# Performance work log

Measured on AMD Instinct MI355X. Metric: run time of the kernel, lower is better.

## Reference

```python
import jax, jax.numpy as jnp
import numpy as np
from jax.ops import segment_sum, segment_max

N_NODES = 16384
N_EDGES = 262144
NODE_DIM = 480
HIDDEN = 256
OUT_DIM = 128
HEADS = 4
N_GRAPHS = 256


def setup_inputs() -> dict:
    key = jax.random.key(0)
    ks = jax.random.split(key, 40)
    p = {}
    p['x'] = jax.random.normal(ks[0], (N_NODES, NODE_DIM), jnp.float32)
    p['edge_index'] = jax.random.randint(ks[1], (2, N_EDGES), 0, N_NODES)
    p['edge_attr'] = jax.random.uniform(ks[2], (N_EDGES, 1), dtype=jnp.float32)
    p['batch'] = jnp.sort(jax.random.randint(ks[3], (N_NODES,), 0, N_GRAPHS))
    p['num_graphs'] = N_GRAPHS
    def w(k, shape):
        return jax.random.normal(k, shape, jnp.float32) * 0.05
    i = 4
    for l, (din, h, c) in zip((1, 2, 3), [(NODE_DIM, HEADS, HIDDEN // HEADS), (HIDDEN, HEADS, HIDDEN // HEADS), (HIDDEN, 1, OUT_DIM)]):
        dout = h * c
        p[f'Wl{l}'] = w(ks[i], (din, dout)); i += 1
        p[f'bl{l}'] = jnp.zeros((dout,), jnp.float32)
        p[f'Wr{l}'] = w(ks[i], (din, dout)); i += 1
        p[f'br{l}'] = jnp.zeros((dout,), jnp.float32)
        p[f'We{l}'] = w(ks[i], (1, dout)); i += 1
        p[f'att{l}'] = w(ks[i], (h, c)); i += 1
        p[f'bo{l}'] = jnp.zeros((dout,), jnp.float32)
    for l, d in [(1, HIDDEN), (2, HIDDEN), (3, OUT_DIM)]:
        p[f'g{l}'] = jnp.ones((d,), jnp.float32)
        p[f'b{l}'] = jnp.zeros((d,), jnp.float32)
    p['Wres'] = w(ks[i], (NODE_DIM, HIDDEN))
    return p


def _layer_norm(x, g, b):
    mu = x.mean(-1, keepdims=True)
    v = ((x - mu) ** 2).mean(-1, keepdims=True)
    return (x - mu) * jax.lax.rsqrt(v + 1e-5) * g + b


def _gatv2(x, src, dst, ea, Wl, bl, Wr, br, We, att, bias):
    # PyG GATv2Conv, eval mode (dropout off), add_self_loops=True, fill_value='mean'
    N = x.shape[0]
    H, C = att.shape
    # self-loop edge attr = scatter-mean of incoming edge attrs per node
    deg = segment_sum(jnp.ones((src.shape[0],), x.dtype), dst, num_segments=N)
    loop_ea = segment_sum(ea, dst, num_segments=N) / jnp.maximum(deg, 1.0)[:, None]
    ar = jnp.arange(N, dtype=src.dtype)
    src2 = jnp.concatenate([src, ar])
    dst2 = jnp.concatenate([dst, ar])
    ea2 = jnp.concatenate([ea, loop_ea], axis=0)
    xl = (x @ Wl + bl).reshape(N, H, C)
    xr = (x @ Wr + br).reshape(N, H, C)
    e = (ea2 @ We).reshape(-1, H, C)
    m = jax.nn.leaky_relu(xl[src2] + xr[dst2] + e, 0.2)  # [E', H, C]
    alpha = jnp.einsum('ehc,hc->eh', m, att)
    amax = segment_max(alpha, dst2, num_segments=N)  # [N, H]; every node has a self loop
    ex = jnp.exp(alpha - amax[dst2])
    denom = segment_sum(ex, dst2, num_segments=N)
    a = ex / denom[dst2]
    out = segment_sum(a[:, :, None] * xl[src2], dst2, num_segments=N)  # [N, H, C]
    return out.reshape(N, H * C) + bias


def _forward(x, edge_attr, params, edge_index, batch, num_graphs):
    (Wl1, bl1, Wr1, br1, We1, att1, bo1,
     Wl2, bl2, Wr2, br2, We2, att2, bo2,
     Wl3, bl3, Wr3, br3, We3, att3, bo3,
     g1, b1, g2, b2, g3, b3, Wres) = params
    src, dst = edge_index[0], edge_index[1]
    gelu = lambda t: jax.nn.gelu(t, approximate=False)
    h = gelu(_layer_norm(_gatv2(x, src, dst, edge_attr, Wl1, bl1, Wr1, br1, We1, att1, bo1), g1, b1))
    h = h + x @ Wres
    h2 = gelu(_layer_norm(_gatv2(h, src, dst, edge_attr, Wl2, bl2, Wr2, br2, We2, att2, bo2), g2, b2))
    h2 = h2 + h
    h3 = _layer_norm(_gatv2(h2, src, dst, edge_attr, Wl3, bl3, Wr3, br3, We3, att3, bo3), g3, b3)
    # global mean pool over graphs
    sums = segment_sum(h3, batch, num_segments=num_graphs)
    cnt = segment_sum(jnp.ones((h3.shape[0],), h3.dtype), batch, num_segments=num_graphs)
    return sums / jnp.maximum(cnt, 1.0)[:, None]


def reference(x, edge_index, edge_attr, batch, num_graphs,
              Wl1, bl1, Wr1, br1, We1, att1, bo1,
              Wl2, bl2, Wr2, br2, We2, att2, bo2,
              Wl3, bl3, Wr3, br3, We3, att3, bo3,
              g1, b1, g2, b2, g3, b3, Wres):
    params = (Wl1, bl1, Wr1, br1, We1, att1, bo1,
              Wl2, bl2, Wr2, br2, We2, att2, bo2,
              Wl3, bl3, Wr3, br3, We3, att3, bo3,
              g1, b1, g2, b2, g3, b3, Wres)
    return _forward(x, edge_attr, params, edge_index, batch, num_graphs)
```

## Files before the change

kernel.cpp:

```cpp
#include <hip/hip_runtime.h>
#include <hip/hip_bf16.h>
#include <math.h>

#define NN 16384
#define NE 262144
#define KDIM1 480
#define DHID 256
#define DOUT3 128
#define NG 256

typedef short bf16x8 __attribute__((ext_vector_type(8)));
typedef float f32x4 __attribute__((ext_vector_type(4)));

#define LOG2E 1.44269504088896340736f

__device__ __forceinline__ unsigned short f2bf(float f) {
  unsigned u = __float_as_uint(f);
  unsigned r = (u + 0x7fffu + ((u >> 16) & 1u)) >> 16;
  return (unsigned short)r;
}
__device__ __forceinline__ float bf2f(unsigned short u) {
  return __uint_as_float((unsigned)u << 16);
}

__device__ __forceinline__ void gload_lds16(const void* g, void* l) {
  __builtin_amdgcn_global_load_lds((const __attribute__((address_space(1))) void*)g,
                                   (__attribute__((address_space(3))) void*)l,
                                   16, 0, 0);
}


__global__ __launch_bounds__(256) void k_edge_count(const int* __restrict__ ei,
                                                    const float* __restrict__ ea,
                                                    int* __restrict__ deg,
                                                    float* __restrict__ easum) {
  int e = blockIdx.x * 256 + threadIdx.x;
  if (e >= NE) return;
  int d = ei[NE + e];
  atomicAdd(&deg[d], 1);
  atomicAdd(&easum[d], ea[e]);
}

__global__ __launch_bounds__(1024) void k_scan(const int* __restrict__ deg,
                                               float* __restrict__ easum,
                                               int* __restrict__ offs,
                                               int* __restrict__ cursor) {
  __shared__ int sums[1024];
  int t = threadIdx.x;
  int base = t * 16;
  int local[16];
  int s = 0;
#pragma unroll
  for (int i = 0; i < 16; ++i) { local[i] = deg[base + i]; s += local[i]; }
  sums[t] = s;
  __syncthreads();
  for (int d = 1; d < 1024; d <<= 1) {
    int v = (t >= d) ? sums[t - d] : 0;
    __syncthreads();
    sums[t] += v;
    __syncthreads();
  }
  int prefix = (t == 0) ? 0 : sums[t - 1];
#pragma unroll
  for (int i = 0; i < 16; ++i) {
    offs[base + i] = prefix;
    cursor[base + i] = prefix;
    prefix += local[i];
  }
  if (t == 1023) offs[NN] = prefix;
#pragma unroll
  for (int i = 0; i < 16; ++i) {
    easum[base + i] = easum[base + i] / fmaxf((float)local[i], 1.f);
  }
}

__global__ __launch_bounds__(256) void k_fill_csr(const int* __restrict__ ei,
                                                  const float* __restrict__ ea,
                                                  int* __restrict__ cursor,
                                                  int* __restrict__ csr_src,
                                                  float* __restrict__ csr_ea) {
  int e = blockIdx.x * 256 + threadIdx.x;
  if (e >= NE) return;
  int s = ei[e];
  int d = ei[NE + e];
  int pos = atomicAdd(&cursor[d], 1);
  csr_src[pos] = s;
  csr_ea[pos] = ea[e];
}


#define PREP_S0 (NN * KDIM1 / 4)
#define PREP_S1 (2 * DHID * KDIM1)
#define PREP_S2 (DHID * KDIM1)
#define PREP_S3 (2 * DHID * DHID)
#define PREP_S4 (2 * DOUT3 * DHID)
#define PREP_TOTAL (PREP_S0 + PREP_S1 + PREP_S2 + PREP_S3 + PREP_S4)

__global__ __launch_bounds__(256) void k_prep(
    const float* __restrict__ x,
    const float* __restrict__ Wl1, const float* __restrict__ Wr1,
    const float* __restrict__ Wres,
    const float* __restrict__ Wl2, const float* __restrict__ Wr2,
    const float* __restrict__ Wl3, const float* __restrict__ Wr3,
    unsigned short* __restrict__ actb0, unsigned short* __restrict__ Wc1,
    unsigned short* __restrict__ Wrs, unsigned short* __restrict__ Wc2,
    unsigned short* __restrict__ Wc3) {
  int idx = blockIdx.x * 256 + threadIdx.x;
  if (idx < PREP_S0) {
    int i = idx * 4;
    float4 v = *(const float4*)&x[i];
    ushort4 o;
    o.x = f2bf(v.x); o.y = f2bf(v.y); o.z = f2bf(v.z); o.w = f2bf(v.w);
    *(ushort4*)&actb0[i] = o;
    return;
  }
  idx -= PREP_S0;
  if (idx < PREP_S1) {
    int n = idx / KDIM1, k = idx % KDIM1;
    float v = (n < DHID) ? Wl1[(size_t)k * DHID + n] : Wr1[(size_t)k * DHID + (n - DHID)];
    Wc1[idx] = f2bf(v);
    return;
  }
  idx -= PREP_S1;
  if (idx < PREP_S2) {
    int n = idx / KDIM1, k = idx % KDIM1;
    Wrs[idx] = f2bf(Wres[(size_t)k * DHID + n]);
    return;
  }
  idx -= PREP_S2;
  if (idx < PREP_S3) {
    int n = idx / DHID, k = idx % DHID;
    float v = (n < DHID) ? Wl2[(size_t)k * DHID + n] : Wr2[(size_t)k * DHID + (n - DHID)];
    Wc2[idx] = f2bf(v);
    return;
  }
  idx -= PREP_S3;
  if (idx < PREP_S4) {
    int n = idx / DHID, k = idx % DHID;
    float v = (n < DOUT3) ? Wl3[(size_t)k * DOUT3 + n] : Wr3[(size_t)k * DOUT3 + (n - DOUT3)];
    Wc3[idx] = f2bf(v);
  }
}


#define GEMM_CORE128(A_, Bt_, K_)                                                \
  __shared__ short As[128 * 32];                                                 \
  __shared__ short Bs[128 * 32];                                                 \
  int t = threadIdx.x;                                                           \
  int w = t >> 6;                                                                \
  int lane = t & 63;                                                             \
  int bm = blockIdx.y * 128;                                                     \
  int bn = blockIdx.x * 128;                                                     \
  int wr = w >> 1, wc = w & 1;                                                   \
  const short* Ag0 = A_ + (size_t)(bm + w * 16 + (lane >> 2)) * K_ + (lane & 3) * 8;        \
  const short* Ag1 = A_ + (size_t)(bm + 64 + w * 16 + (lane >> 2)) * K_ + (lane & 3) * 8;   \
  const short* Bg0 = Bt_ + (size_t)(bn + w * 16 + (lane >> 2)) * K_ + (lane & 3) * 8;       \
  const short* Bg1 = Bt_ + (size_t)(bn + 64 + w * 16 + (lane >> 2)) * K_ + (lane & 3) * 8;  \
  short* Al0 = &As[w * 16 * 32];                                                 \
  short* Al1 = &As[(64 + w * 16) * 32];                                          \
  short* Bl0 = &Bs[w * 16 * 32];                                                 \
  short* Bl1 = &Bs[(64 + w * 16) * 32];                                          \
  f32x4 acc[4][4] = {};                                                          \
  for (int k0 = 0; k0 < K_; k0 += 32) {                                          \
    gload_lds16(Ag0, Al0);                                                       \
    gload_lds16(Ag1, Al1);                                                       \
    gload_lds16(Bg0, Bl0);                                                       \
    gload_lds16(Bg1, Bl1);                                                       \
    Ag0 += 32; Ag1 += 32; Bg0 += 32; Bg1 += 32;                                  \
    __syncthreads();                                                             \
    bf16x8 af[4], bfv[4];                                                        \
    _Pragma("unroll")                                                            \
    for (int mi = 0; mi < 4; ++mi)                                               \
      af[mi] = *(const bf16x8*)&As[(wr * 64 + mi * 16 + (lane & 15)) * 32 + (lane >> 4) * 8]; \
    _Pragma("unroll")                                                            \
    for (int ni = 0; ni < 4; ++ni)                                               \
      bfv[ni] = *(const bf16x8*)&Bs[(wc * 64 + ni * 16 + (lane & 15)) * 32 + (lane >> 4) * 8]; \
    _Pragma("unroll")                                                            \
    for (int mi = 0; mi < 4; ++mi)                                               \
      _Pragma("unroll")                                                          \
      for (int ni = 0; ni < 4; ++ni)                                             \
        acc[mi][ni] = __builtin_amdgcn_mfma_f32_16x16x32_bf16(af[mi], bfv[ni], acc[mi][ni], 0, 0, 0); \
    __syncthreads();                                                             \
  }                                                                              \
  int col = lane & 15;                                                           \
  int row4 = (lane >> 4) * 4;

__global__ __launch_bounds__(256) void gemm_lr(const short* __restrict__ A,
                                               const short* __restrict__ Wt,
                                               const float* __restrict__ bl,
                                               const float* __restrict__ br,
                                               unsigned short* __restrict__ xlb,
                                               unsigned short* __restrict__ xrb,
                                               int K, int NH) {
  GEMM_CORE128(A, Wt, K)
  bool right = (bn >= NH);
  unsigned short* outp = right ? xrb : xlb;
  const float* bias = right ? br : bl;
  int cbase = right ? bn - NH : bn;
#pragma unroll
  for (int mi = 0; mi < 4; ++mi) {
#pragma unroll
    for (int ni = 0; ni < 4; ++ni) {
      f32x4 a = acc[mi][ni];
      int gc = cbase + wc * 64 + ni * 16 + col;
      float bv = bias[gc];
#pragma unroll
      for (int r = 0; r < 4; ++r) {
        int gr = bm + wr * 64 + mi * 16 + row4 + r;
        outp[(size_t)gr * NH + gc] = f2bf(a[r] + bv);
      }
    }
  }
}

__global__ __launch_bounds__(256) void gemm_res(const short* __restrict__ A,
                                                const short* __restrict__ Wt,
                                                float* __restrict__ Cf,
                                                unsigned short* __restrict__ outb,
                                                int K, int N) {
  GEMM_CORE128(A, Wt, K)
#pragma unroll
  for (int mi = 0; mi < 4; ++mi) {
#pragma unroll
    for (int ni = 0; ni < 4; ++ni) {
      f32x4 a = acc[mi][ni];
      int gc = bn + wc * 64 + ni * 16 + col;
#pragma unroll
      for (int r = 0; r < 4; ++r) {
        int gr = bm + wr * 64 + mi * 16 + row4 + r;
        size_t o = (size_t)gr * N + gc;
        float v = a[r] + Cf[o];
        Cf[o] = v;
        outb[o] = f2bf(v);
      }
    }
  }
}


template<int D, int H, bool GELU_, bool RES_, bool WF32, bool WBF16>
__global__ __launch_bounds__(256) void gat_fused(
    const unsigned short* __restrict__ xlb, const unsigned short* __restrict__ xrb,
    const float* __restrict__ We, const float* __restrict__ att,
    const float* __restrict__ bo,
    const int* __restrict__ offs, const int* __restrict__ csr_src,
    const float* __restrict__ csr_ea, const float* __restrict__ loop_ea,
    const float* __restrict__ g, const float* __restrict__ bln,
    const float* __restrict__ res,
    float* __restrict__ outf, unsigned short* __restrict__ outb) {
  constexpr int P = D / 64;
  constexpr int C = D / H;
  constexpr int GROUP = C / P;
  int n = (blockIdx.x * blockDim.x + threadIdx.x) >> 6;
  int lane = threadIdx.x & 63;
  if (n >= NN) return;
  int d0 = lane * P;

  float wev[P], attv[P], xrv[P];
  if constexpr (P == 4) {
    *(float4*)wev = *(const float4*)&We[d0];
    *(float4*)attv = *(const float4*)&att[d0];
    ushort4 u = *(const ushort4*)&xrb[(size_t)n * D + d0];
    xrv[0] = bf2f(u.x); xrv[1] = bf2f(u.y); xrv[2] = bf2f(u.z); xrv[3] = bf2f(u.w);
  } else {
    *(float2*)wev = *(const float2*)&We[d0];
    *(float2*)attv = *(const float2*)&att[d0];
    ushort2 u = *(const ushort2*)&xrb[(size_t)n * D + d0];
    xrv[0] = bf2f(u.x); xrv[1] = bf2f(u.y);
  }
#pragma unroll
  for (int p = 0; p < P; ++p) attv[p] *= LOG2E;

#define GATHER(dst, srcidx)                                                  \
  {                                                                          \
    if constexpr (P == 4) {                                                  \
      ushort4 u_ = *(const ushort4*)&xlb[(size_t)(srcidx) * D + d0];         \
      dst[0] = bf2f(u_.x); dst[1] = bf2f(u_.y);                              \
      dst[2] = bf2f(u_.z); dst[3] = bf2f(u_.w);                              \
    } else {                                                                 \
      ushort2 u_ = *(const ushort2*)&xlb[(size_t)(srcidx) * D + d0];         \
      dst[0] = bf2f(u_.x); dst[1] = bf2f(u_.y);                              \
    }                                                                        \
  }

#define ALPHA(out_, xv_, eav_)                                               \
  {                                                                          \
    float partial_ = 0.f;                                                    \
    _Pragma("unroll")                                                        \
    for (int p = 0; p < P; ++p) {                                            \
      float s_ = xv_[p] + xrv[p] + (eav_) * wev[p];                          \
      s_ = fmaxf(s_, 0.2f * s_);                                             \
      partial_ = fmaf(s_, attv[p], partial_);                                \
    }                                                                        \
    _Pragma("unroll")                                                        \
    for (int w_ = 1; w_ < GROUP; w_ <<= 1) partial_ += __shfl_xor(partial_, w_, 64); \
    out_ = partial_;                                                         \
  }

  float acc[P];
  float xs[P];
  GATHER(xs, n)
  float m;
  ALPHA(m, xs, loop_ea[n])
  float l = 1.f;
#pragma unroll
  for (int p = 0; p < P; ++p) acc[p] = xs[p];

  int beg = offs[n];
  int cnt = offs[n + 1] - beg;
  int sbeg = __builtin_amdgcn_readfirstlane(beg);
  int scnt = __builtin_amdgcn_readfirstlane(cnt);

  int e = 0;
  for (; e + 4 <= scnt; e += 4) {
    int src0 = csr_src[sbeg + e];
    int src1 = csr_src[sbeg + e + 1];
    int src2 = csr_src[sbeg + e + 2];
    int src3 = csr_src[sbeg + e + 3];
    float ea0 = csr_ea[sbeg + e];
    float ea1 = csr_ea[sbeg + e + 1];
    float ea2 = csr_ea[sbeg + e + 2];
    float ea3 = csr_ea[sbeg + e + 3];
    float xv0[P], xv1[P], xv2[P], xv3[P];
    GATHER(xv0, src0)
    GATHER(xv1, src1)
    GATHER(xv2, src2)
    GATHER(xv3, src3)
    float a0, a1, a2, a3;
    ALPHA(a0, xv0, ea0)
    ALPHA(a1, xv1, ea1)
    ALPHA(a2, xv2, ea2)
    ALPHA(a3, xv3, ea3)
    float nm = fmaxf(fmaxf(m, fmaxf(a0, a1)), fmaxf(a2, a3));
    float sc = exp2f(m - nm);
    float pe0 = exp2f(a0 - nm);
    float pe1 = exp2f(a1 - nm);
    float pe2 = exp2f(a2 - nm);
    float pe3 = exp2f(a3 - nm);
    l = fmaf(l, sc, (pe0 + pe1) + (pe2 + pe3));
#pragma unroll
    for (int p = 0; p < P; ++p)
      acc[p] = fmaf(acc[p], sc,
                    fmaf(pe0, xv0[p], fmaf(pe1, xv1[p], fmaf(pe2, xv2[p], pe3 * xv3[p]))));
    m = nm;
  }
  for (; e < scnt; ++e) {
    int src0 = csr_src[sbeg + e];
    float ea0 = csr_ea[sbeg + e];
    float xv0[P];
    GATHER(xv0, src0)
    float a0;
    ALPHA(a0, xv0, ea0)
    float nm = fmaxf(m, a0);
    float sc = exp2f(m - nm);
    float pe0 = exp2f(a0 - nm);
    l = fmaf(l, sc, pe0);
#pragma unroll
    for (int p = 0; p < P; ++p) acc[p] = fmaf(acc[p], sc, pe0 * xv0[p]);
    m = nm;
  }
#undef GATHER
#undef ALPHA

  float inv = 1.f / l;
  float y[P];
#pragma unroll
  for (int p = 0; p < P; ++p) y[p] = fmaf(acc[p], inv, bo[d0 + p]);

  float s = 0.f, s2 = 0.f;
#pragma unroll
  for (int p = 0; p < P; ++p) { s += y[p]; s2 = fmaf(y[p], y[p], s2); }
#pragma unroll
  for (int w = 1; w < 64; w <<= 1) {
    s += __shfl_xor(s, w, 64);
    s2 += __shfl_xor(s2, w, 64);
  }
  float mu = s * (1.f / D);
  float var = s2 * (1.f / D) - mu * mu;
  float rr = rsqrtf(var + 1e-5f);

  float z[P];
#pragma unroll
  for (int p = 0; p < P; ++p) {
    float v = (y[p] - mu) * rr * g[d0 + p] + bln[d0 + p];
    if (GELU_) v = 0.5f * v * (1.f + erff(v * 0.70710678118654752f));
    if (RES_) v += res[(size_t)n * D + d0 + p];
    z[p] = v;
  }
  if (WF32) {
    float* orow = outf + (size_t)n * D;
    if constexpr (P == 4) *(float4*)&orow[d0] = *(float4*)z;
    else                  *(float2*)&orow[d0] = *(float2*)z;
  }
  if (WBF16) {
    unsigned short* orow = outb + (size_t)n * D;
    if constexpr (P == 4) {
      ushort4 o; o.x = f2bf(z[0]); o.y = f2bf(z[1]); o.z = f2bf(z[2]); o.w = f2bf(z[3]);
      *(ushort4*)&orow[d0] = o;
    } else {
      ushort2 o; o.x = f2bf(z[0]); o.y = f2bf(z[1]);
      *(ushort2*)&orow[d0] = o;
    }
  }
}


__device__ __forceinline__ int lower_bound_i(const int* arr, int n, int val) {
  int lo = 0, hi = n;
  while (lo < hi) {
    int mid = (lo + hi) >> 1;
    if (arr[mid] < val) lo = mid + 1; else hi = mid;
  }
  return lo;
}

__global__ __launch_bounds__(128) void k_pool(const float* __restrict__ h3,
                                              const int* __restrict__ batch,
                                              float* __restrict__ out) {
  int gidx = blockIdx.x;
  int d = threadIdx.x;
  int lo = lower_bound_i(batch, NN, gidx);
  int hi = lower_bound_i(batch, NN, gidx + 1);
  float s = 0.f;
  for (int n = lo; n < hi; ++n) s += h3[(size_t)n * DOUT3 + d];
  int cnt = hi - lo;
  out[gidx * DOUT3 + d] = s / fmaxf((float)cnt, 1.f);
}


extern "C" void kernel_launch(void* const* d_in, const int* in_sizes, int n_in,
                              void* d_out, int out_size, void* d_ws, size_t ws_size,
                              hipStream_t stream) {
  const float* x   = (const float*)d_in[0];
  const int*   ei  = (const int*)d_in[1];
  const float* ea  = (const float*)d_in[2];
  const int*   bat = (const int*)d_in[3];
  const float* Wl1 = (const float*)d_in[5];  const float* bl1 = (const float*)d_in[6];
  const float* Wr1 = (const float*)d_in[7];  const float* br1 = (const float*)d_in[8];
  const float* We1 = (const float*)d_in[9];  const float* at1 = (const float*)d_in[10];
  const float* bo1 = (const float*)d_in[11];
  const float* Wl2 = (const float*)d_in[12]; const float* bl2 = (const float*)d_in[13];
  const float* Wr2 = (const float*)d_in[14]; const float* br2 = (const float*)d_in[15];
  const float* We2 = (const float*)d_in[16]; const float* at2 = (const float*)d_in[17];
  const float* bo2 = (const float*)d_in[18];
  const float* Wl3 = (const float*)d_in[19]; const float* bl3 = (const float*)d_in[20];
  const float* Wr3 = (const float*)d_in[21]; const float* br3 = (const float*)d_in[22];
  const float* We3 = (const float*)d_in[23]; const float* at3 = (const float*)d_in[24];
  const float* bo3 = (const float*)d_in[25];
  const float* g1 = (const float*)d_in[26]; const float* b1 = (const float*)d_in[27];
  const float* g2 = (const float*)d_in[28]; const float* b2 = (const float*)d_in[29];
  const float* g3 = (const float*)d_in[30]; const float* b3 = (const float*)d_in[31];
  const float* Wres = (const float*)d_in[32];
  float* out = (float*)d_out;

  char* ws = (char*)d_ws;
  size_t off = 0;
  int*   deg    = (int*)(ws + off); off += NN * 4;
  float* easum  = (float*)(ws + off); off += NN * 4;
  size_t zero_bytes = off;
  unsigned short* xlb = (unsigned short*)(ws + off); off += (size_t)NN * DHID * 2;
  unsigned short* xrb = (unsigned short*)(ws + off); off += (size_t)NN * DHID * 2;
  float* hb = (float*)(ws + off); off += (size_t)NN * DHID * 4;
  float* h3 = (float*)(ws + off); off += (size_t)NN * DOUT3 * 4;
  unsigned short* actb0 = (unsigned short*)(ws + off); off += (size_t)NN * KDIM1 * 2;
  unsigned short* actb1 = (unsigned short*)(ws + off); off += (size_t)NN * DHID * 2;
  int*   offs   = (int*)(ws + off); off += (NN + 1) * 4 + 60;
  int*   cursor = (int*)(ws + off); off += NN * 4;
  int*   csr_src = (int*)(ws + off); off += (size_t)NE * 4;
  float* csr_ea  = (float*)(ws + off); off += (size_t)NE * 4;
  unsigned short* Wc1 = (unsigned short*)(ws + off); off += (size_t)2 * DHID * KDIM1 * 2;
  unsigned short* Wrs = (unsigned short*)(ws + off); off += (size_t)DHID * KDIM1 * 2;
  unsigned short* Wc2 = (unsigned short*)(ws + off); off += (size_t)2 * DHID * DHID * 2;
  unsigned short* Wc3 = (unsigned short*)(ws + off); off += (size_t)2 * DOUT3 * DHID * 2;

  hipMemsetAsync(deg, 0, zero_bytes, stream);
  k_edge_count<<<NE / 256, 256, 0, stream>>>(ei, ea, deg, easum);
  k_scan<<<1, 1024, 0, stream>>>(deg, easum, offs, cursor);
  k_fill_csr<<<NE / 256, 256, 0, stream>>>(ei, ea, cursor, csr_src, csr_ea);
  k_prep<<<PREP_TOTAL / 256, 256, 0, stream>>>(x, Wl1, Wr1, Wres, Wl2, Wr2, Wl3, Wr3,
                                               actb0, Wc1, Wrs, Wc2, Wc3);

  dim3 blk(256);
  int nwave_blocks = NN / 4;

  gemm_lr<<<dim3(2 * DHID / 128, NN / 128), blk, 0, stream>>>(
      (const short*)actb0, (const short*)Wc1, bl1, br1, xlb, xrb, KDIM1, DHID);
  gat_fused<DHID, 4, true, false, true, false><<<nwave_blocks, blk, 0, stream>>>(
      xlb, xrb, We1, at1, bo1, offs, csr_src, csr_ea, easum, g1, b1, nullptr, hb, nullptr);
  gemm_res<<<dim3(DHID / 128, NN / 128), blk, 0, stream>>>(
      (const short*)actb0, (const short*)Wrs, hb, actb1, KDIM1, DHID);

  gemm_lr<<<dim3(2 * DHID / 128, NN / 128), blk, 0, stream>>>(
      (const short*)actb1, (const short*)Wc2, bl2, br2, xlb, xrb, DHID, DHID);
  gat_fused<DHID, 4, true, true, false, true><<<nwave_blocks, blk, 0, stream>>>(
      xlb, xrb, We2, at2, bo2, offs, csr_src, csr_ea, easum, g2, b2, hb, nullptr, actb1);

  gemm_lr<<<dim3(2 * DOUT3 / 128, NN / 128), blk, 0, stream>>>(
      (const short*)actb1, (const short*)Wc3, bl3, br3, xlb, xrb, DHID, DOUT3);
  gat_fused<DOUT3, 1, false, false, true, false><<<nwave_blocks, blk, 0, stream>>>(
      xlb, xrb, We3, at3, bo3, offs, csr_src, csr_ea, easum, g3, b3, nullptr, h3, nullptr);

  k_pool<<<NG, 128, 0, stream>>>(h3, bat, out);
}
```

Baseline: 263.7 us.

## Fuse residual GEMM into layer-1 GEMM and pooling into layer-3 GAT

The Wres projection is concatenated with Wl1/Wr1 so a single GEMM over the 480-wide input produces xl, xr and the fp32 residual. Layer-1 GAT now adds that residual itself and writes the bf16 activations, which removes the separate gemm_res pass and its second read of actb0. The global mean pool is folded into the layer-3 GAT epilogue through atomic adds scaled by precomputed inverse graph counts, and h3 is no longer written. The cost is heavy atomic contention on the 256x128 output, plus atomic summation order that is not deterministic.

```diff
diff --git a/kernel.cpp b/kernel.cpp
--- a/kernel.cpp
+++ b/kernel.cpp
@@ -27,6 +27,15 @@
   __builtin_amdgcn_global_load_lds((const __attribute__((address_space(1))) void*)g,
                                    (__attribute__((address_space(3))) void*)l,
                                    16, 0, 0);
+}
+
+__device__ __forceinline__ int lower_bound_i(const int* arr, int n, int val) {
+  int lo = 0, hi = n;
+  while (lo < hi) {
+    int mid = (lo + hi) >> 1;
+    if (arr[mid] < val) lo = mid + 1; else hi = mid;
+  }
+  return lo;
 }
 
 
@@ -44,7 +53,9 @@
 __global__ __launch_bounds__(1024) void k_scan(const int* __restrict__ deg,
                                                float* __restrict__ easum,
                                                int* __restrict__ offs,
-                                               int* __restrict__ cursor) {
+                                               int* __restrict__ cursor,
+                                               const int* __restrict__ bat,
+                                               float* __restrict__ ginv) {
   __shared__ int sums[1024];
   int t = threadIdx.x;
   int base = t * 16;
@@ -71,6 +82,11 @@
 #pragma unroll
   for (int i = 0; i < 16; ++i) {
     easum[base + i] = easum[base + i] / fmaxf((float)local[i], 1.f);
+  }
+  if (t < NG) {
+    int lo = lower_bound_i(bat, NN, t);
+    int hi = lower_bound_i(bat, NN, t + 1);
+    ginv[t] = 1.f / fmaxf((float)(hi - lo), 1.f);
   }
 }
 
@@ -90,11 +106,10 @@
 
 
 #define PREP_S0 (NN * KDIM1 / 4)
-#define PREP_S1 (2 * DHID * KDIM1)
-#define PREP_S2 (DHID * KDIM1)
-#define PREP_S3 (2 * DHID * DHID)
-#define PREP_S4 (2 * DOUT3 * DHID)
-#define PREP_TOTAL (PREP_S0 + PREP_S1 + PREP_S2 + PREP_S3 + PREP_S4)
+#define PREP_S1 (3 * DHID * KDIM1)
+#define PREP_S2 (2 * DHID * DHID)
+#define PREP_S3 (2 * DOUT3 * DHID)
+#define PREP_TOTAL (PREP_S0 + PREP_S1 + PREP_S2 + PREP_S3)
 
 __global__ __launch_bounds__(256) void k_prep(
     const float* __restrict__ x,
@@ -102,9 +117,8 @@
     const float* __restrict__ Wres,
     const float* __restrict__ Wl2, const float* __restrict__ Wr2,
     const float* __restrict__ Wl3, const float* __restrict__ Wr3,
-    unsigned short* __restrict__ actb0, unsigned short* __restrict__ Wc1,
-    unsigned short* __restrict__ Wrs, unsigned short* __restrict__ Wc2,
-    unsigned short* __restrict__ Wc3) {
+    unsigned short* __restrict__ actb0, unsigned short* __restrict__ Wc1e,
+    unsigned short* __restrict__ Wc2, unsigned short* __restrict__ Wc3) {
   int idx = blockIdx.x * 256 + threadIdx.x;
   if (idx < PREP_S0) {
     int i = idx * 4;
@@ -117,25 +131,22 @@
   idx -= PREP_S0;
   if (idx < PREP_S1) {
     int n = idx / KDIM1, k = idx % KDIM1;
-    float v = (n < DHID) ? Wl1[(size_t)k * DHID + n] : Wr1[(size_t)k * DHID + (n - DHID)];
-    Wc1[idx] = f2bf(v);
+    float v;
+    if (n < DHID)            v = Wl1[(size_t)k * DHID + n];
+    else if (n < 2 * DHID)   v = Wr1[(size_t)k * DHID + (n - DHID)];
+    else                     v = Wres[(size_t)k * DHID + (n - 2 * DHID)];
+    Wc1e[idx] = f2bf(v);
     return;
   }
   idx -= PREP_S1;
   if (idx < PREP_S2) {
-    int n = idx / KDIM1, k = idx % KDIM1;
-    Wrs[idx] = f2bf(Wres[(size_t)k * DHID + n]);
-    return;
-  }
-  idx -= PREP_S2;
-  if (idx < PREP_S3) {
     int n = idx / DHID, k = idx % DHID;
     float v = (n < DHID) ? Wl2[(size_t)k * DHID + n] : Wr2[(size_t)k * DHID + (n - DHID)];
     Wc2[idx] = f2bf(v);
     return;
   }
-  idx -= PREP_S3;
-  if (idx < PREP_S4) {
+  idx -= PREP_S2;
+  if (idx < PREP_S3) {
     int n = idx / DHID, k = idx % DHID;
     float v = (n < DOUT3) ? Wl3[(size_t)k * DOUT3 + n] : Wr3[(size_t)k * DOUT3 + (n - DOUT3)];
     Wc3[idx] = f2bf(v);
@@ -185,6 +196,43 @@
   int col = lane & 15;                                                           \
   int row4 = (lane >> 4) * 4;
 
+__global__ __launch_bounds__(256) void gemm_lrr(const short* __restrict__ A,
+                                                const short* __restrict__ Wt,
+                                                const float* __restrict__ bl,
+                                                const float* __restrict__ br,
+                                                unsigned short* __restrict__ xlb,
+                                                unsigned short* __restrict__ xrb,
+                                                float* __restrict__ xres,
+                                                int K, int NH) {
+  GEMM_CORE128(A, Wt, K)
+  int seg = bn / NH;
+  int cbase = bn - seg * NH;
+#pragma unroll
+  for (int mi = 0; mi < 4; ++mi) {
+#pragma unroll
+    for (int ni = 0; ni < 4; ++ni) {
+      f32x4 a = acc[mi][ni];
+      int gc = cbase + wc * 64 + ni * 16 + col;
+      if (seg == 2) {
+#pragma unroll
+        for (int r = 0; r < 4; ++r) {
+          int gr = bm + wr * 64 + mi * 16 + row4 + r;
+          xres[(size_t)gr * NH + gc] = a[r];
+        }
+      } else {
+        const float* bias = seg ? br : bl;
+        unsigned short* outp = seg ? xrb : xlb;
+        float bv = bias[gc];
+#pragma unroll
+        for (int r = 0; r < 4; ++r) {
+          int gr = bm + wr * 64 + mi * 16 + row4 + r;
+          outp[(size_t)gr * NH + gc] = f2bf(a[r] + bv);
+        }
+      }
+    }
+  }
+}
+
 __global__ __launch_bounds__(256) void gemm_lr(const short* __restrict__ A,
                                                const short* __restrict__ Wt,
                                                const float* __restrict__ bl,
@@ -213,32 +261,8 @@
   }
 }
 
-__global__ __launch_bounds__(256) void gemm_res(const short* __restrict__ A,
-                                                const short* __restrict__ Wt,
-                                                float* __restrict__ Cf,
-                                                unsigned short* __restrict__ outb,
-                                                int K, int N) {
-  GEMM_CORE128(A, Wt, K)
-#pragma unroll
-  for (int mi = 0; mi < 4; ++mi) {
-#pragma unroll
-    for (int ni = 0; ni < 4; ++ni) {
-      f32x4 a = acc[mi][ni];
-      int gc = bn + wc * 64 + ni * 16 + col;
-#pragma unroll
-      for (int r = 0; r < 4; ++r) {
-        int gr = bm + wr * 64 + mi * 16 + row4 + r;
-        size_t o = (size_t)gr * N + gc;
-        float v = a[r] + Cf[o];
-        Cf[o] = v;
-        outb[o] = f2bf(v);
-      }
-    }
-  }
-}
-
-
-template<int D, int H, bool GELU_, bool RES_, bool WF32, bool WBF16>
+
+template<int D, int H, bool GELU_, bool RES_, bool WF32, bool WBF16, bool POOL>
 __global__ __launch_bounds__(256) void gat_fused(
     const unsigned short* __restrict__ xlb, const unsigned short* __restrict__ xrb,
     const float* __restrict__ We, const float* __restrict__ att,
@@ -247,7 +271,9 @@
     const float* __restrict__ csr_ea, const float* __restrict__ loop_ea,
     const float* __restrict__ g, const float* __restrict__ bln,
     const float* __restrict__ res,
-    float* __restrict__ outf, unsigned short* __restrict__ outb) {
+    float* __restrict__ outf, unsigned short* __restrict__ outb,
+    const int* __restrict__ batch, const float* __restrict__ ginv,
+    float* __restrict__ outp) {
   constexpr int P = D / 64;
   constexpr int C = D / H;
   constexpr int GROUP = C / P;
@@ -402,29 +428,13 @@
       *(ushort2*)&orow[d0] = o;
     }
   }
-}
-
-
-__device__ __forceinline__ int lower_bound_i(const int* arr, int n, int val) {
-  int lo = 0, hi = n;
-  while (lo < hi) {
-    int mid = (lo + hi) >> 1;
-    if (arr[mid] < val) lo = mid + 1; else hi = mid;
-  }
-  return lo;
-}
-
-__global__ __launch_bounds__(128) void k_pool(const float* __restrict__ h3,
-                                              const int* __restrict__ batch,
-                                              float* __restrict__ out) {
-  int gidx = blockIdx.x;
-  int d = threadIdx.x;
-  int lo = lower_bound_i(batch, NN, gidx);
-  int hi = lower_bound_i(batch, NN, gidx + 1);
-  float s = 0.f;
-  for (int n = lo; n < hi; ++n) s += h3[(size_t)n * DOUT3 + d];
-  int cnt = hi - lo;
-  out[gidx * DOUT3 + d] = s / fmaxf((float)cnt, 1.f);
+  if (POOL) {
+    int gr = batch[n];
+    float wgt = ginv[gr];
+#pragma unroll
+    for (int p = 0; p < P; ++p)
+      atomicAdd(&outp[gr * D + d0 + p], z[p] * wgt);
+  }
 }
 
 
@@ -460,45 +470,45 @@
   size_t zero_bytes = off;
   unsigned short* xlb = (unsigned short*)(ws + off); off += (size_t)NN * DHID * 2;
   unsigned short* xrb = (unsigned short*)(ws + off); off += (size_t)NN * DHID * 2;
-  float* hb = (float*)(ws + off); off += (size_t)NN * DHID * 4;
-  float* h3 = (float*)(ws + off); off += (size_t)NN * DOUT3 * 4;
+  float* hb   = (float*)(ws + off); off += (size_t)NN * DHID * 4;
+  float* xres = (float*)(ws + off); off += (size_t)NN * DHID * 4;
   unsigned short* actb0 = (unsigned short*)(ws + off); off += (size_t)NN * KDIM1 * 2;
   unsigned short* actb1 = (unsigned short*)(ws + off); off += (size_t)NN * DHID * 2;
   int*   offs   = (int*)(ws + off); off += (NN + 1) * 4 + 60;
   int*   cursor = (int*)(ws + off); off += NN * 4;
+  float* ginv   = (float*)(ws + off); off += NG * 4;
   int*   csr_src = (int*)(ws + off); off += (size_t)NE * 4;
   float* csr_ea  = (float*)(ws + off); off += (size_t)NE * 4;
-  unsigned short* Wc1 = (unsigned short*)(ws + off); off += (size_t)2 * DHID * KDIM1 * 2;
-  unsigned short* Wrs = (unsigned short*)(ws + off); off += (size_t)DHID * KDIM1 * 2;
-  unsigned short* Wc2 = (unsigned short*)(ws + off); off += (size_t)2 * DHID * DHID * 2;
-  unsigned short* Wc3 = (unsigned short*)(ws + off); off += (size_t)2 * DOUT3 * DHID * 2;
+  unsigned short* Wc1e = (unsigned short*)(ws + off); off += (size_t)3 * DHID * KDIM1 * 2;
+  unsigned short* Wc2  = (unsigned short*)(ws + off); off += (size_t)2 * DHID * DHID * 2;
+  unsigned short* Wc3  = (unsigned short*)(ws + off); off += (size_t)2 * DOUT3 * DHID * 2;
 
   hipMemsetAsync(deg, 0, zero_bytes, stream);
+  hipMemsetAsync(out, 0, (size_t)NG * DOUT3 * 4, stream);
   k_edge_count<<<NE / 256, 256, 0, stream>>>(ei, ea, deg, easum);
-  k_scan<<<1, 1024, 0, stream>>>(deg, easum, offs, cursor);
+  k_scan<<<1, 1024, 0, stream>>>(deg, easum, offs, cursor, bat, ginv);
   k_fill_csr<<<NE / 256, 256, 0, stream>>>(ei, ea, cursor, csr_src, csr_ea);
-  k_prep<<<PREP_TOTAL / 256, 256, 0, stream>>>(x, Wl1, Wr1, Wres, Wl2, Wr2, Wl3, Wr3,
-                                               actb0, Wc1, Wrs, Wc2, Wc3);
+  k_prep<<<(PREP_TOTAL + 255) / 256, 256, 0, stream>>>(x, Wl1, Wr1, Wres, Wl2, Wr2, Wl3, Wr3,
+                                                       actb0, Wc1e, Wc2, Wc3);
 
   dim3 blk(256);
   int nwave_blocks = NN / 4;
 
-  gemm_lr<<<dim3(2 * DHID / 128, NN / 128), blk, 0, stream>>>(
-      (const short*)actb0, (const short*)Wc1, bl1, br1, xlb, xrb, KDIM1, DHID);
-  gat_fused<DHID, 4, true, false, true, false><<<nwave_blocks, blk, 0, stream>>>(
-      xlb, xrb, We1, at1, bo1, offs, csr_src, csr_ea, easum, g1, b1, nullptr, hb, nullptr);
-  gemm_res<<<dim3(DHID / 128, NN / 128), blk, 0, stream>>>(
-      (const short*)actb0, (const short*)Wrs, hb, actb1, KDIM1, DHID);
+  gemm_lrr<<<dim3(3 * DHID / 128, NN / 128), blk, 0, stream>>>(
+      (const short*)actb0, (const short*)Wc1e, bl1, br1, xlb, xrb, xres, KDIM1, DHID);
+  gat_fused<DHID, 4, true, true, true, true, false><<<nwave_blocks, blk, 0, stream>>>(
+      xlb, xrb, We1, at1, bo1, offs, csr_src, csr_ea, easum, g1, b1, xres, hb, actb1,
+      nullptr, nullptr, nullptr);
 
   gemm_lr<<<dim3(2 * DHID / 128, NN / 128), blk, 0, stream>>>(
       (const short*)actb1, (const short*)Wc2, bl2, br2, xlb, xrb, DHID, DHID);
-  gat_fused<DHID, 4, true, true, false, true><<<nwave_blocks, blk, 0, stream>>>(
-      xlb, xrb, We2, at2, bo2, offs, csr_src, csr_ea, easum, g2, b2, hb, nullptr, actb1);
+  gat_fused<DHID, 4, true, true, false, true, false><<<nwave_blocks, blk, 0, stream>>>(
+      xlb, xrb, We2, at2, bo2, offs, csr_src, csr_ea, easum, g2, b2, hb, nullptr, actb1,
+      nullptr, nullptr, nullptr);
 
   gemm_lr<<<dim3(2 * DOUT3 / 128, NN / 128), blk, 0, stream>>>(
       (const short*)actb1, (const short*)Wc3, bl3, br3, xlb, xrb, DHID, DOUT3);
-  gat_fused<DOUT3, 1, false, false, true, false><<<nwave_blocks, blk, 0, stream>>>(
-      xlb, xrb, We3, at3, bo3, offs, csr_src, csr_ea, easum, g3, b3, nullptr, h3, nullptr);
-
-  k_pool<<<NG, 128, 0, stream>>>(h3, bat, out);
-}
+  gat_fused<DOUT3, 1, false, false, false, false, true><<<nwave_blocks, blk, 0, stream>>>(
+      xlb, xrb, We3, at3, bo3, offs, csr_src, csr_ea, easum, g3, b3, nullptr, nullptr, nullptr,
+      bat, ginv, out);
+}
```

Measured after the change: 223.6 us. 1.18x faster.
